# Optimization experiments

Hardware: AMD Instinct MI355X
Metric: run time of the kernel (lower is better)

The kernel has to match this reference:

```python
import jax, jax.numpy as jnp
import numpy as np
from jax import lax

K = 11  # kernel_size
THRESH = 0.2  # focus_threshold default
DN = ('NCHW', 'OIHW', 'NCHW')


def conv3(x, w, b):
    # 3x3 conv, stride 1, SAME padding (padding=1 in torch)
    return lax.conv_general_dilated(x, w, (1, 1), 'SAME', dimension_numbers=DN) + b[None, :, None, None]


def apply_separable_filters(rgb, kh, kv, k):
    # rgb [B,3,H,W]; kh, kv [B,k,H,W] softmaxed per-pixel 1D kernels
    pad = k // 2
    B, C, H, W = rgb.shape
    # horizontal pass: gather k horizontally-shifted views, weight by kh
    xp = jnp.pad(rgb, ((0, 0), (0, 0), (0, 0), (pad, pad)))
    ph = jnp.stack([xp[:, :, :, i:i + W] for i in range(k)], axis=2)  # [B,3,k,H,W]
    h = jnp.einsum('bckhw,bkhw->bchw', ph, kh)
    # vertical pass
    hp = jnp.pad(h, ((0, 0), (0, 0), (pad, pad), (0, 0)))
    pv = jnp.stack([hp[:, :, i:i + H, :] for i in range(k)], axis=2)  # [B,3,k,H,W]
    return jnp.einsum('bckhw,bkhw->bchw', pv, kv)


def get_depth_mask(depth, threshold):
    # binary in-focus mask: pixels closer than threshold stay sharp
    return (depth > threshold).astype(depth.dtype)


def setup_inputs() -> dict:
    key = jax.random.key(0)
    ks = jax.random.split(key, 18)
    B, H, W = 8, 256, 256
    s = 0.05
    f32 = jnp.float32
    inp = {
        'rgb': jax.random.uniform(ks[0], (B, 3, H, W), f32),
        'depth': jax.random.uniform(ks[1], (B, 1, H, W), f32),
        'w1': jax.random.normal(ks[2], (64, 4, 3, 3), f32) * s, 'b1': jnp.zeros(64, f32),
        'w2': jax.random.normal(ks[3], (64, 64, 3, 3), f32) * s, 'b2': jnp.zeros(64, f32),
        'w3': jax.random.normal(ks[4], (128, 64, 3, 3), f32) * s, 'b3': jnp.zeros(128, f32),
        'w4': jax.random.normal(ks[5], (128, 128, 3, 3), f32) * s, 'b4': jnp.zeros(128, f32),
        'w5': jax.random.normal(ks[6], (64, 128, 3, 3), f32) * s, 'b5': jnp.zeros(64, f32),
        'wh': jax.random.normal(ks[7], (K, 64, 3, 3), f32) * s, 'bh': jnp.zeros(K, f32),
        'wv': jax.random.normal(ks[8], (K, 64, 3, 3), f32) * s, 'bv': jnp.zeros(K, f32),
    }
    return inp


def reference(rgb, depth, w1, b1, w2, b2, w3, b3, w4, b4, w5, b5, wh, bh, wv, bv):
    x = jnp.concatenate([rgb, depth], axis=1)  # [B,4,H,W]
    f = jax.nn.relu(conv3(x, w1, b1))
    f = jax.nn.relu(conv3(f, w2, b2))
    f = jax.nn.relu(conv3(f, w3, b3))
    f = jax.nn.relu(conv3(f, w4, b4))
    f = jax.nn.relu(conv3(f, w5, b5))
    kh = jax.nn.softmax(conv3(f, wh, bh), axis=1)
    kv = jax.nn.softmax(conv3(f, wv, bv), axis=1)
    blurred = apply_separable_filters(rgb, kh, kv, K)
    mask = get_depth_mask(depth, THRESH)
    final = mask * rgb + (1.0 - mask) * blurred
    return (final, blurred, kh, kv, mask)
```

## Files before the change

### kernel.cpp

```cpp
#include <hip/hip_runtime.h>
#include <hip/hip_bf16.h>
#include <math.h>

#define HH 256
#define WW 256
#define HW (HH*WW)
#define BB 8

typedef __hip_bfloat16 bf16;
typedef __attribute__((ext_vector_type(8))) short short8;
typedef __attribute__((ext_vector_type(4))) float f32x4;
typedef __attribute__((ext_vector_type(16))) float f32x16;

#define AS1 __attribute__((address_space(1)))
#define AS3 __attribute__((address_space(3)))


template<int CO, int CI>
__global__ __launch_bounds__(256) void reorder_w_cl(const float* __restrict__ w,
                                                    bf16* __restrict__ wr)
{
    int idx = blockIdx.x * 256 + threadIdx.x;
    if (idx >= 9 * CO * CI) return;
    int j    = idx & 7;
    int lane = (idx >> 3) & 63;
    int nt   = (idx >> 9) % (CO / 32);
    int rest = idx / (512 * (CO / 32));
    int ks   = rest & 1;
    int tt   = (rest >> 1) % 9;
    int kc   = rest / 18;
    int co = nt * 32 + (lane & 31);
    int ci = kc * 32 + ks * 16 + (lane >> 5) * 8 + j;
    wr[idx] = __float2bfloat16(w[((size_t)co * CI + ci) * 9 + tt]);
}

__global__ __launch_bounds__(256) void reorder_w_head2(const float* __restrict__ wh,
                                                       const float* __restrict__ wv,
                                                       bf16* __restrict__ wr)
{
    int idx = blockIdx.x * 256 + threadIdx.x;
    if (idx >= 9 * 32 * 64) return;
    int ci = idx % 64;
    int co = (idx / 64) % 32;
    int t  = idx / (64 * 32);
    const float* src = (co < 16) ? wh : wv;
    int c = co & 15;
    float v = (c < 11) ? src[((size_t)c * 64 + ci) * 9 + t] : 0.0f;
    wr[idx] = __float2bfloat16(v);
}

template<int ROWS, int TPB>
__device__ __forceinline__ void zero_oob(bf16* __restrict__ s0,
                                         bf16* __restrict__ s1,
                                         int tid, int x0, int y0)
{
    constexpr int UNITS = (ROWS + 2) * 264;
    const short8 z8 = {0,0,0,0,0,0,0,0};
    for (int e = tid; e < UNITS; e += TPB) {
        int row = e / 264, rem = e - row * 264;
        int px = rem >> 2;
        int yy = y0 - 1 + row, xx = x0 - 1 + px;
        if (yy < 0 || yy >= HH || xx < 0 || xx >= WW) {
            *(short8*)(s0 + (size_t)e * 8) = z8;
            *(short8*)(s1 + (size_t)e * 8) = z8;
        }
    }
}

template<int CIN, int ROWS, int TPB>
__device__ __forceinline__ void stage_async(const bf16* __restrict__ in_i,
                                            bf16* __restrict__ slab,
                                            int tid, int x0, int y0, int k0)
{
    constexpr int UNITS = (ROWS + 2) * 264;
    const int lane = tid & 63;
    const int wb   = tid - lane;
    for (int base = wb; base < UNITS; base += TPB) {
        int e = base + lane;
        int row = e / 264, rem = e - row * 264;
        int px = rem >> 2, slot = rem & 3;
        int seg = slot ^ ((px >> 1) & 3);
        int yy = y0 - 1 + row, xx = x0 - 1 + px;
        bool ok = (e < UNITS) && (yy >= 0) && (yy < HH) && (xx >= 0) && (xx < WW);
        if (ok) {
            const bf16* g = in_i + ((size_t)(yy * WW + xx)) * CIN + k0 + seg * 8;
            __builtin_amdgcn_global_load_lds((const AS1 void*)g,
                                             (AS3 void*)(slab + (size_t)base * 8),
                                             16, 0, 0);
        }
    }
}

template<int COC>
__global__ __launch_bounds__(256) void conv3x3_first(const float* __restrict__ rgb,
                                                     const float* __restrict__ depth,
                                                     const float* __restrict__ w,
                                                     const float* __restrict__ bias,
                                                     bf16* __restrict__ out, int b0)
{
    const int tid = threadIdx.x;
    const int img = blockIdx.y >> 6;
    const int b   = b0 + img;
    const int x = blockIdx.x * 64 + (tid & 63);
    const int y = (blockIdx.y & 63) * 4 + (tid >> 6);
    const int cog = blockIdx.z * COC;

    const bool vy0 = (y > 0), vy2 = (y < HH - 1);
    const bool vx0 = (x > 0), vx2 = (x < WW - 1);
    bool val[9];
    int  off[9];
    {
        int t = 0;
        for (int dy = -1; dy <= 1; ++dy)
            for (int dx = -1; dx <= 1; ++dx) {
                val[t] = (dy < 0 ? vy0 : (dy > 0 ? vy2 : true)) &&
                         (dx < 0 ? vx0 : (dx > 0 ? vx2 : true));
                off[t] = dy * WW + dx;
                ++t;
            }
    }

    float acc[COC];
#pragma unroll
    for (int j = 0; j < COC; ++j) acc[j] = bias[cog + j];

    const int p0 = y * WW + x;
#pragma unroll
    for (int ci = 0; ci < 4; ++ci) {
        const float* p = (ci < 3) ? (rgb + ((size_t)(b * 3 + ci)) * HW + p0)
                                  : (depth + (size_t)b * HW + p0);
        float v[9];
#pragma unroll
        for (int t = 0; t < 9; ++t)
            v[t] = val[t] ? p[off[t]] : 0.0f;

        const float* wp = w + ((size_t)cog * 4 + ci) * 9;
#pragma unroll
        for (int j = 0; j < COC; ++j) {
            const float* wj = wp + (size_t)j * 4 * 9;
#pragma unroll
            for (int t = 0; t < 9; ++t)
                acc[j] = fmaf(wj[t], v[t], acc[j]);
        }
    }

    bf16* op = out + (size_t)img * HW * 64 + (size_t)p0 * 64 + cog;
#pragma unroll
    for (int g = 0; g < COC / 8; ++g) {
        short8 s;
#pragma unroll
        for (int j = 0; j < 8; ++j) {
            bf16 h = __float2bfloat16(fmaxf(acc[g * 8 + j], 0.0f));
            s[j] = *reinterpret_cast<short*>(&h);
        }
        *(short8*)(op + g * 8) = s;
    }
}

template<int CIN, int COUT, int WPB>
__global__ __launch_bounds__(256, WPB) void conv_mfma_v12(const bf16* __restrict__ in,
                                                          const bf16* __restrict__ wrb,
                                                          const float* __restrict__ bias,
                                                          bf16* __restrict__ out)
{
    constexpr int NCH  = CIN / 32;
    constexpr int NTT  = COUT / 64;
    constexpr int NTOT = COUT / 32;
    constexpr int SLAB = 6 * 66 * 32;
    __shared__ bf16 slab[2 * SLAB];

    const int tid  = threadIdx.x;
    const int lane = tid & 63;
    const int wv   = tid >> 6;
    const int ng   = wv & 1;
    const int rg   = wv >> 1;
    const int ln31 = lane & 31;
    const int oct  = lane >> 5;
    const int img  = blockIdx.y >> 6;
    const int x0   = blockIdx.x * 64;
    const int y0   = (blockIdx.y & 63) * 4;

    const bf16* in_i  = in  + (size_t)img * HW * CIN;
    bf16*       out_i = out + (size_t)img * HW * COUT;

    f32x16 acc[4][NTT];
#pragma unroll
    for (int mt = 0; mt < 4; ++mt)
#pragma unroll
        for (int nt = 0; nt < NTT; ++nt)
#pragma unroll
            for (int j = 0; j < 16; ++j) acc[mt][nt][j] = 0.0f;

    zero_oob<4, 256>(slab, slab + SLAB, tid, x0, y0);
    stage_async<CIN, 4, 256>(in_i, slab, tid, x0, y0, 0);

    int cur = 0;
    for (int kc = 0; kc < NCH; ++kc) {
        __syncthreads();
        if (kc + 1 < NCH)
            stage_async<CIN, 4, 256>(in_i, slab + (size_t)(cur ^ 1) * SLAB,
                                     tid, x0, y0, (kc + 1) * 32);

        const bf16* sb = slab + (size_t)cur * SLAB;
#pragma unroll
        for (int t = 0; t < 9; ++t) {
            const int dy = t / 3 - 1, dx = t % 3 - 1;
#pragma unroll
            for (int ks = 0; ks < 2; ++ks) {
                short8 a[4];
#pragma unroll
                for (int mt = 0; mt < 4; ++mt) {
                    const int srow = 2 * rg + (mt >> 1) + dy + 1;
                    const int px   = (mt & 1) * 32 + ln31 + dx + 1;
                    const int slot = (ks * 2 + oct) ^ ((px >> 1) & 3);
                    a[mt] = *(const short8*)(sb + (srow * 66 + px) * 32 + slot * 8);
                }
#pragma unroll
                for (int nt = 0; nt < NTT; ++nt) {
                    const int gnt = ng * NTT + nt;
                    short8 bfr = *(const short8*)(wrb
                        + ((size_t)((((kc * 9 + t) * 2 + ks) * NTOT + gnt) * 64 + lane)) * 8);
#pragma unroll
                    for (int mt = 0; mt < 4; ++mt)
                        acc[mt][nt] = __builtin_amdgcn_mfma_f32_32x32x16_bf16(
                                          a[mt], bfr, acc[mt][nt], 0, 0, 0);
                }
            }
        }
        cur ^= 1;
    }

#pragma unroll
    for (int nt = 0; nt < NTT; ++nt) {
        const int co = (ng * NTT + nt) * 32 + ln31;
        const float bb = bias[co];
#pragma unroll
        for (int mt = 0; mt < 4; ++mt) {
            const int r  = 2 * rg + (mt >> 1);
            const int xb = x0 + (mt & 1) * 32;
#pragma unroll
            for (int j = 0; j < 16; ++j) {
                const int m = (j & 3) + 8 * (j >> 2) + 4 * oct;
                const float v = fmaxf(acc[mt][nt][j] + bb, 0.0f);
                out_i[((size_t)(y0 + r) * WW + (xb + m)) * COUT + co] = __float2bfloat16(v);
            }
        }
    }
}

__global__ __launch_bounds__(256, 2) void head_mfma2(const bf16* __restrict__ in,
                                                     const bf16* __restrict__ wrp,
                                                     const float* __restrict__ bh,
                                                     const float* __restrict__ bv,
                                                     float* __restrict__ kh_base,
                                                     float* __restrict__ kv_base,
                                                     int b0)
{
    constexpr int SLABH = 6 * 66 * 32;
    __shared__ bf16  slab[2 * SLABH];
    __shared__ float smx[4][64][17];

    const int tid  = threadIdx.x;
    const int lane = tid & 63;
    const int wv   = tid >> 6;
    const int m    = lane & 15;
    const int q    = lane >> 4;
    const int img  = blockIdx.y >> 6;
    const int x0   = blockIdx.x * 64;
    const int y0   = (blockIdx.y & 63) * 4;
    const int y    = y0 + wv;

    const bf16* in_i = in + (size_t)img * HW * 64;

    f32x4 acc[4][2];
#pragma unroll
    for (int f = 0; f < 4; ++f) { acc[f][0] = (f32x4){0.f,0.f,0.f,0.f}; acc[f][1] = (f32x4){0.f,0.f,0.f,0.f}; }

    zero_oob<4, 256>(slab, slab + SLABH, tid, x0, y0);
    stage_async<64, 4, 256>(in_i, slab, tid, x0, y0, 0);

    int cur = 0;
    for (int kc = 0; kc < 2; ++kc) {
        __syncthreads();
        if (kc == 0)
            stage_async<64, 4, 256>(in_i, slab + SLABH, tid, x0, y0, 32);

        const bf16* sb = slab + (size_t)cur * SLABH;
        const int k0 = kc * 32;
#pragma unroll
        for (int t = 0; t < 9; ++t) {
            const int dy = t / 3 - 1, dx = t % 3 - 1;
            const int srow = wv + dy + 1;
            const bf16* wt = wrp + (size_t)t * 32 * 64 + (size_t)m * 64 + k0 + q * 8;
            short8 b0f = *(const short8*)(wt);
            short8 b1f = *(const short8*)(wt + 16 * 64);
#pragma unroll
            for (int f = 0; f < 4; ++f) {
                const int px = f * 16 + m + dx + 1;
                const int slot = q ^ ((px >> 1) & 3);
                short8 a = *(const short8*)(sb + (srow * 66 + px) * 32 + slot * 8);
                acc[f][0] = __builtin_amdgcn_mfma_f32_16x16x32_bf16(a, b0f, acc[f][0], 0, 0, 0);
                acc[f][1] = __builtin_amdgcn_mfma_f32_16x16x32_bf16(a, b1f, acc[f][1], 0, 0, 0);
            }
        }
        cur ^= 1;
    }

#pragma unroll
    for (int head = 0; head < 2; ++head) {
        const float* bias = head ? bv : bh;
        const float bb = (m < 11) ? bias[m] : 0.0f;
#pragma unroll
        for (int f = 0; f < 4; ++f)
#pragma unroll
            for (int r = 0; r < 4; ++r)
                smx[wv][f * 16 + q * 4 + r][m] = acc[f][head][r] + bb;

        float v[11];
#pragma unroll
        for (int j = 0; j < 11; ++j) v[j] = smx[wv][lane][j];
        float mx = v[0];
#pragma unroll
        for (int j = 1; j < 11; ++j) mx = fmaxf(mx, v[j]);
        float s = 0.0f;
#pragma unroll
        for (int j = 0; j < 11; ++j) { v[j] = expf(v[j] - mx); s += v[j]; }
        const float inv = 1.0f / s;

        float* op = (head ? kv_base : kh_base) + (size_t)(b0 + img) * 11 * HW
                    + (size_t)y * WW + x0 + lane;
#pragma unroll
        for (int j = 0; j < 11; ++j)
            op[(size_t)j * HW] = v[j] * inv;
    }
}

__global__ __launch_bounds__(256) void hpass(const float* __restrict__ rgb,
                                             const float* __restrict__ kh,
                                             float* __restrict__ h)
{
    int idx = blockIdx.x * 256 + threadIdx.x;
    int b = idx >> 16;
    int p = idx & (HW - 1);
    int y = p >> 8;
    int x = p & 255;

    float kw[11];
#pragma unroll
    for (int i = 0; i < 11; ++i) kw[i] = kh[((size_t)(b * 11 + i)) * HW + p];

#pragma unroll
    for (int c = 0; c < 3; ++c) {
        const float* rp = rgb + ((size_t)(b * 3 + c)) * HW + (size_t)y * WW;
        float s = 0.0f;
#pragma unroll
        for (int i = 0; i < 11; ++i) {
            int xx = x + i - 5;
            if (xx >= 0 && xx < WW) s = fmaf(kw[i], rp[xx], s);
        }
        h[((size_t)(b * 3 + c)) * HW + p] = s;
    }
}

__global__ __launch_bounds__(256) void vpass_compose(const float* __restrict__ h,
                                                     const float* __restrict__ kv,
                                                     const float* __restrict__ rgb,
                                                     const float* __restrict__ depth,
                                                     float* __restrict__ fin,
                                                     float* __restrict__ blur,
                                                     float* __restrict__ masko)
{
    int idx = blockIdx.x * 256 + threadIdx.x;
    int b = idx >> 16;
    int p = idx & (HW - 1);
    int y = p >> 8;
    int x = p & 255;

    float kw[11];
#pragma unroll
    for (int i = 0; i < 11; ++i) kw[i] = kv[((size_t)(b * 11 + i)) * HW + p];

    float d = depth[idx];
    float mk = (d > 0.2f) ? 1.0f : 0.0f;
    masko[idx] = mk;

#pragma unroll
    for (int c = 0; c < 3; ++c) {
        const float* hp = h + ((size_t)(b * 3 + c)) * HW + x;
        float s = 0.0f;
#pragma unroll
        for (int i = 0; i < 11; ++i) {
            int yy = y + i - 5;
            if (yy >= 0 && yy < HH) s = fmaf(kw[i], hp[(size_t)yy * WW], s);
        }
        size_t o = ((size_t)(b * 3 + c)) * HW + p;
        blur[o] = s;
        fin[o] = mk * rgb[o] + (1.0f - mk) * s;
    }
}

extern "C" void kernel_launch(void* const* d_in, const int* in_sizes, int n_in,
                              void* d_out, int out_size, void* d_ws, size_t ws_size,
                              hipStream_t stream)
{
    const float* rgb   = (const float*)d_in[0];
    const float* depth = (const float*)d_in[1];
    const float* w1 = (const float*)d_in[2];  const float* b1 = (const float*)d_in[3];
    const float* w2 = (const float*)d_in[4];  const float* b2 = (const float*)d_in[5];
    const float* w3 = (const float*)d_in[6];  const float* b3 = (const float*)d_in[7];
    const float* w4 = (const float*)d_in[8];  const float* b4 = (const float*)d_in[9];
    const float* w5 = (const float*)d_in[10]; const float* b5 = (const float*)d_in[11];
    const float* wh = (const float*)d_in[12]; const float* bh = (const float*)d_in[13];
    const float* wv = (const float*)d_in[14]; const float* bv = (const float*)d_in[15];

    float* out    = (float*)d_out;
    float* fin_o  = out;
    float* blur_o = out + 1572864;
    float* kh_o   = out + 3145728;
    float* kv_o   = out + 8912896;
    float* mask_o = out + 14680064;

    const size_t perG = (size_t)HW * 2 * (128 + 64 + 128);
    const size_t wsz  = (size_t)1 * 1024 * 1024;
    int G = 1;
    if (ws_size >= 8 * perG + wsz) G = 8;
    else if (ws_size >= 4 * perG + wsz) G = 4;
    else if (ws_size >= 2 * perG + wsz) G = 2;

    char* ws = (char*)d_ws;
    const size_t szA = (size_t)G * HW * 128 * 2;
    const size_t szB = (size_t)G * HW * 64 * 2;
    const size_t szC = (size_t)G * HW * 128 * 2;
    bf16* bufA = (bf16*)ws;
    bf16* bufB = (bf16*)(ws + szA);
    bf16* bufC = (bf16*)(ws + szA + szB);
    float* hbuf = (float*)bufC;

    bf16* w2r  = (bf16*)(ws + szA + szB + szC);
    bf16* w3r  = w2r + 9 * 64 * 64;
    bf16* w4r  = w3r + 9 * 128 * 64;
    bf16* w5r  = w4r + 9 * 128 * 128;
    bf16* whvr = w5r + 9 * 64 * 128;

    dim3 blk(256);

    reorder_w_cl<64, 64>  <<<dim3((9*64*64   + 255) / 256), blk, 0, stream>>>(w2, w2r);
    reorder_w_cl<128, 64> <<<dim3((9*128*64  + 255) / 256), blk, 0, stream>>>(w3, w3r);
    reorder_w_cl<128, 128><<<dim3((9*128*128 + 255) / 256), blk, 0, stream>>>(w4, w4r);
    reorder_w_cl<64, 128> <<<dim3((9*64*128  + 255) / 256), blk, 0, stream>>>(w5, w5r);
    reorder_w_head2       <<<dim3((9*32*64   + 255) / 256), blk, 0, stream>>>(wh, wv, whvr);

    for (int b0 = 0; b0 < BB; b0 += G) {
        conv3x3_first<16><<<dim3(4, 64 * G, 4), blk, 0, stream>>>(rgb, depth, w1, b1, bufA, b0);
        conv_mfma_v12<64, 64, 3>  <<<dim3(4, 64 * G), blk, 0, stream>>>(bufA, w2r, b2, bufB);
        conv_mfma_v12<64, 128, 2> <<<dim3(4, 64 * G), blk, 0, stream>>>(bufB, w3r, b3, bufC);
        conv_mfma_v12<128, 128, 2><<<dim3(4, 64 * G), blk, 0, stream>>>(bufC, w4r, b4, bufA);
        conv_mfma_v12<128, 64, 3> <<<dim3(4, 64 * G), blk, 0, stream>>>(bufA, w5r, b5, bufB);
        head_mfma2<<<dim3(4, 64 * G), blk, 0, stream>>>(bufB, whvr, bh, bv, kh_o, kv_o, b0);
    }

    hpass<<<dim3(2048), blk, 0, stream>>>(rgb, kh_o, hbuf);
    vpass_compose<<<dim3(2048), blk, 0, stream>>>(hbuf, kv_o, rgb, depth,
                                                  fin_o, blur_o, mask_o);
}
```

Measured before the change: 767.9 us.

## Reuse A fragments across dy taps and lane-major head weight layout

Adds a conv_mfma_v13 variant that loads four slab rows of A fragments per dx/ks and reuses them across the three dy taps. This cuts redundant LDS reads compared with per-tap loading, at the cost of more registers holding fragments. It is used for the two 64-output-channel layers. The head weights are also reordered into a lane-major layout so each lane's B fragment comes from one contiguous, coalesced load.

After: 747.7 us. 2.6% less time.

```diff
diff --git a/kernel.cpp b/kernel.cpp
--- a/kernel.cpp
+++ b/kernel.cpp
@@ -34,15 +34,19 @@
     wr[idx] = __float2bfloat16(w[((size_t)co * CI + ci) * 9 + tt]);
 }
 
-__global__ __launch_bounds__(256) void reorder_w_head2(const float* __restrict__ wh,
-                                                       const float* __restrict__ wv,
-                                                       bf16* __restrict__ wr)
+__global__ __launch_bounds__(256) void reorder_w_head2_lm(const float* __restrict__ wh,
+                                                          const float* __restrict__ wv,
+                                                          bf16* __restrict__ wr)
 {
     int idx = blockIdx.x * 256 + threadIdx.x;
-    if (idx >= 9 * 32 * 64) return;
-    int ci = idx % 64;
-    int co = (idx / 64) % 32;
-    int t  = idx / (64 * 32);
+    if (idx >= 2 * 9 * 2 * 64 * 8) return;
+    int j    = idx & 7;
+    int lane = (idx >> 3) & 63;
+    int fr   = (idx >> 9) & 1;
+    int t    = (idx >> 10) % 9;
+    int kc   = (idx >> 10) / 9;
+    int co   = fr * 16 + (lane & 15);
+    int ci   = kc * 32 + (lane >> 4) * 8 + j;
     const float* src = (co < 16) ? wh : wv;
     int c = co & 15;
     float v = (c < 11) ? src[((size_t)c * 64 + ci) * 9 + t] : 0.0f;
@@ -248,6 +252,102 @@
     }
 }
 
+template<int CIN, int COUT, int WPB>
+__global__ __launch_bounds__(256, WPB) void conv_mfma_v13(const bf16* __restrict__ in,
+                                                          const bf16* __restrict__ wrb,
+                                                          const float* __restrict__ bias,
+                                                          bf16* __restrict__ out)
+{
+    constexpr int NCH  = CIN / 32;
+    constexpr int NTT  = COUT / 64;
+    constexpr int NTOT = COUT / 32;
+    constexpr int SLAB = 6 * 66 * 32;
+    __shared__ bf16 slab[2 * SLAB];
+
+    const int tid  = threadIdx.x;
+    const int lane = tid & 63;
+    const int wv   = tid >> 6;
+    const int ng   = wv & 1;
+    const int rg   = wv >> 1;
+    const int ln31 = lane & 31;
+    const int oct  = lane >> 5;
+    const int img  = blockIdx.y >> 6;
+    const int x0   = blockIdx.x * 64;
+    const int y0   = (blockIdx.y & 63) * 4;
+
+    const bf16* in_i  = in  + (size_t)img * HW * CIN;
+    bf16*       out_i = out + (size_t)img * HW * COUT;
+
+    f32x16 acc[4][NTT];
+#pragma unroll
+    for (int mt = 0; mt < 4; ++mt)
+#pragma unroll
+        for (int nt = 0; nt < NTT; ++nt)
+#pragma unroll
+            for (int j = 0; j < 16; ++j) acc[mt][nt][j] = 0.0f;
+
+    zero_oob<4, 256>(slab, slab + SLAB, tid, x0, y0);
+    stage_async<CIN, 4, 256>(in_i, slab, tid, x0, y0, 0);
+
+    int cur = 0;
+    for (int kc = 0; kc < NCH; ++kc) {
+        __syncthreads();
+        if (kc + 1 < NCH)
+            stage_async<CIN, 4, 256>(in_i, slab + (size_t)(cur ^ 1) * SLAB,
+                                     tid, x0, y0, (kc + 1) * 32);
+
+        const bf16* sb = slab + (size_t)cur * SLAB;
+#pragma unroll
+        for (int dxi = 0; dxi < 3; ++dxi) {
+            const int dx = dxi - 1;
+#pragma unroll
+            for (int ks = 0; ks < 2; ++ks) {
+                short8 af[4][2];
+#pragma unroll
+                for (int s = 0; s < 4; ++s)
+#pragma unroll
+                    for (int mx = 0; mx < 2; ++mx) {
+                        const int px   = mx * 32 + ln31 + dx + 1;
+                        const int slot = (ks * 2 + oct) ^ ((px >> 1) & 3);
+                        af[s][mx] = *(const short8*)(sb + ((2 * rg + s) * 66 + px) * 32 + slot * 8);
+                    }
+#pragma unroll
+                for (int dyi = 0; dyi < 3; ++dyi) {
+                    const int t = dyi * 3 + dxi;
+#pragma unroll
+                    for (int nt = 0; nt < NTT; ++nt) {
+                        const int gnt = ng * NTT + nt;
+                        short8 bfr = *(const short8*)(wrb
+                            + ((size_t)((((kc * 9 + t) * 2 + ks) * NTOT + gnt) * 64 + lane)) * 8);
+#pragma unroll
+                        for (int mt = 0; mt < 4; ++mt)
+                            acc[mt][nt] = __builtin_amdgcn_mfma_f32_32x32x16_bf16(
+                                              af[(mt >> 1) + dyi][mt & 1], bfr, acc[mt][nt], 0, 0, 0);
+                    }
+                }
+            }
+        }
+        cur ^= 1;
+    }
+
+#pragma unroll
+    for (int nt = 0; nt < NTT; ++nt) {
+        const int co = (ng * NTT + nt) * 32 + ln31;
+        const float bb = bias[co];
+#pragma unroll
+        for (int mt = 0; mt < 4; ++mt) {
+            const int r  = 2 * rg + (mt >> 1);
+            const int xb = x0 + (mt & 1) * 32;
+#pragma unroll
+            for (int j = 0; j < 16; ++j) {
+                const int m = (j & 3) + 8 * (j >> 2) + 4 * oct;
+                const float v = fmaxf(acc[mt][nt][j] + bb, 0.0f);
+                out_i[((size_t)(y0 + r) * WW + (xb + m)) * COUT + co] = __float2bfloat16(v);
+            }
+        }
+    }
+}
+
 __global__ __launch_bounds__(256, 2) void head_mfma2(const bf16* __restrict__ in,
                                                      const bf16* __restrict__ wrp,
                                                      const float* __restrict__ bh,
@@ -286,14 +386,12 @@
             stage_async<64, 4, 256>(in_i, slab + SLABH, tid, x0, y0, 32);
 
         const bf16* sb = slab + (size_t)cur * SLABH;
-        const int k0 = kc * 32;
 #pragma unroll
         for (int t = 0; t < 9; ++t) {
             const int dy = t / 3 - 1, dx = t % 3 - 1;
             const int srow = wv + dy + 1;
-            const bf16* wt = wrp + (size_t)t * 32 * 64 + (size_t)m * 64 + k0 + q * 8;
-            short8 b0f = *(const short8*)(wt);
-            short8 b1f = *(const short8*)(wt + 16 * 64);
+            short8 b0f = *(const short8*)(wrp + ((size_t)(((kc * 9 + t) * 2 + 0) * 64 + lane)) * 8);
+            short8 b1f = *(const short8*)(wrp + ((size_t)(((kc * 9 + t) * 2 + 1) * 64 + lane)) * 8);
 #pragma unroll
             for (int f = 0; f < 4; ++f) {
                 const int px = f * 16 + m + dx + 1;
@@ -448,14 +546,14 @@
     reorder_w_cl<128, 64> <<<dim3((9*128*64  + 255) / 256), blk, 0, stream>>>(w3, w3r);
     reorder_w_cl<128, 128><<<dim3((9*128*128 + 255) / 256), blk, 0, stream>>>(w4, w4r);
     reorder_w_cl<64, 128> <<<dim3((9*64*128  + 255) / 256), blk, 0, stream>>>(w5, w5r);
-    reorder_w_head2       <<<dim3((9*32*64   + 255) / 256), blk, 0, stream>>>(wh, wv, whvr);
+    reorder_w_head2_lm    <<<dim3((18432     + 255) / 256), blk, 0, stream>>>(wh, wv, whvr);
 
     for (int b0 = 0; b0 < BB; b0 += G) {
         conv3x3_first<16><<<dim3(4, 64 * G, 4), blk, 0, stream>>>(rgb, depth, w1, b1, bufA, b0);
-        conv_mfma_v12<64, 64, 3>  <<<dim3(4, 64 * G), blk, 0, stream>>>(bufA, w2r, b2, bufB);
+        conv_mfma_v13<64, 64, 3>  <<<dim3(4, 64 * G), blk, 0, stream>>>(bufA, w2r, b2, bufB);
         conv_mfma_v12<64, 128, 2> <<<dim3(4, 64 * G), blk, 0, stream>>>(bufB, w3r, b3, bufC);
         conv_mfma_v12<128, 128, 2><<<dim3(4, 64 * G), blk, 0, stream>>>(bufC, w4r, b4, bufA);
-        conv_mfma_v12<128, 64, 3> <<<dim3(4, 64 * G), blk, 0, stream>>>(bufA, w5r, b5, bufB);
+        conv_mfma_v13<128, 64, 3> <<<dim3(4, 64 * G), blk, 0, stream>>>(bufA, w5r, b5, bufB);
         head_mfma2<<<dim3(4, 64 * G), blk, 0, stream>>>(bufB, whvr, bh, bv, kh_o, kv_o, b0);
     }
 
```
